# Kernel optimization log

Hardware: AMD Instinct MI355X
Metric: run time of the kernel (lower is better)

Reference implementation:

```python
import jax, jax.numpy as jnp
import numpy as np

B, N, DIM = 1, 4096, 512
HEADS, LOCAL_HEADS = 8, 4           # int(8*0.6)=4 local, 4 content
CONTENT_HEADS = HEADS - LOCAL_HEADS
HEAD_DIM = DIM // HEADS             # 64
WINDOW = 64                         # == H == W so window attention is well-formed
TOPK_RATIO = 0.2
SCALE = HEAD_DIM ** -0.5


def _window_partition(x, ws):
    Bb, H, W, C = x.shape
    pad_h = (ws - H % ws) % ws
    pad_w = (ws - W % ws) % ws
    x = jnp.pad(x, ((0, 0), (0, pad_h), (0, pad_w), (0, 0)))
    Hp, Wp = H + pad_h, W + pad_w
    x = x.reshape(Bb, Hp // ws, ws, Wp // ws, ws, C)
    win = x.transpose(0, 1, 3, 2, 4, 5).reshape(-1, ws, ws, C)
    return win, (Hp, Wp)


def _window_unpartition(win, ws, pad_hw, hw):
    Hp, Wp = pad_hw
    H, W = hw
    Bb = win.shape[0] // (Hp * Wp // ws // ws)
    x = win.reshape(Bb, Hp // ws, Wp // ws, ws, ws, -1)
    x = x.transpose(0, 1, 3, 2, 4, 5).reshape(Bb, Hp, Wp, -1)
    return x[:, :H, :W, :]


def setup_inputs() -> dict:
    key = jax.random.key(0)
    ks = jax.random.split(key, 12)
    s = 0.02
    f32 = jnp.float32
    ld = LOCAL_HEADS * HEAD_DIM      # 256
    cd = CONTENT_HEADS * HEAD_DIM    # 256
    return {
        'x': jax.random.normal(ks[0], (B, N, DIM), f32),
        'W_lqkv': jax.random.normal(ks[1], (DIM, 3 * ld), f32) * s,
        'b_lqkv': jnp.zeros((3 * ld,), f32),
        'W_cqkv': jax.random.normal(ks[2], (DIM, 3 * cd), f32) * s,
        'b_cqkv': jnp.zeros((3 * cd,), f32),
        'W_lproj': jax.random.normal(ks[3], (ld, DIM), f32) * s,
        'b_lproj': jnp.zeros((DIM,), f32),
        'W_cproj': jax.random.normal(ks[4], (cd, DIM), f32) * s,
        'b_cproj': jnp.zeros((DIM,), f32),
        'W_s1': jax.random.normal(ks[5], (DIM, DIM // 2), f32) * s,
        'b_s1': jnp.zeros((DIM // 2,), f32),
        'W_s2': jax.random.normal(ks[6], (DIM // 2, 1), f32) * s,
        'b_s2': jnp.zeros((1,), f32),
    }


def reference(x, W_lqkv, b_lqkv, W_cqkv, b_cqkv, W_lproj, b_lproj,
              W_cproj, b_cproj, W_s1, b_s1, W_s2, b_s2):
    Bb, Nn, C = x.shape
    H = W = int(np.sqrt(Nn))

    # ---- local (windowed) attention branch ----
    x_sp = x.reshape(Bb, H, W, C)
    x_win, pad_hw = _window_partition(x_sp, WINDOW)           # (Bw, ws, ws, C)
    Bw, Hw, Ww, _ = x_win.shape
    Nw = Hw * Ww
    xl = x_win.reshape(Bw, Nw, C)
    lqkv = (xl @ W_lqkv + b_lqkv).reshape(Bw, Nw, 3, LOCAL_HEADS, HEAD_DIM)
    lqkv = lqkv.transpose(2, 0, 3, 1, 4)                      # (3, Bw, h, Nw, d)
    lq, lk, lv = lqkv[0], lqkv[1], lqkv[2]
    lattn = jnp.einsum('bhqd,bhkd->bhqk', lq, lk) * SCALE
    lattn = jax.nn.softmax(lattn, axis=-1)
    lo = jnp.einsum('bhqk,bhkd->bhqd', lattn, lv)
    lo = lo.transpose(0, 2, 1, 3).reshape(Bw, Hw, Ww, LOCAL_HEADS * HEAD_DIM)
    lo = _window_unpartition(lo, WINDOW, pad_hw, (H, W)).reshape(Bb, Nn, -1)
    local_x = lo @ W_lproj + b_lproj

    # ---- saliency-gated content-based sparse attention branch ----
    h = jax.nn.gelu(x @ W_s1 + b_s1, approximate=False)
    scores = (h @ W_s2 + b_s2)[..., 0]                        # (B, N)
    K = max(1, int(Nn * TOPK_RATIO))
    _, idx = jax.lax.top_k(scores, K)                         # (B, K)
    mask = jnp.zeros((Bb, Nn), bool).at[jnp.arange(Bb)[:, None], idx].set(True)

    cqkv = (x @ W_cqkv + b_cqkv).reshape(Bb, Nn, 3, CONTENT_HEADS, HEAD_DIM)
    cqkv = cqkv.transpose(2, 0, 3, 1, 4)
    cq, ck, cv = cqkv[0], cqkv[1], cqkv[2]
    cattn = jnp.einsum('bhqd,bhkd->bhqk', cq, ck) * SCALE
    cattn = jnp.where(mask[:, None, None, :], cattn, -jnp.inf)
    cattn = jax.nn.softmax(cattn, axis=-1)
    co = jnp.einsum('bhqk,bhkd->bhqd', cattn, cv)
    co = co.transpose(0, 2, 1, 3).reshape(Bb, Nn, CONTENT_HEADS * HEAD_DIM)
    content_x = co @ W_cproj + b_cproj

    out = local_x + content_x
    attn = jnp.concatenate([lattn.mean(axis=1), cattn.mean(axis=1)], axis=1)
    return out, attn
```

## Files before the change

kernel.cpp:

```cpp
#include <hip/hip_runtime.h>

typedef __bf16 bf16;
typedef __bf16 bf16x8 __attribute__((ext_vector_type(8)));
typedef float  floatx4 __attribute__((ext_vector_type(4)));

#define SCALE 0.125f

__device__ __forceinline__ floatx4 mfma16(bf16x8 a, bf16x8 b, floatx4 c) {
    return __builtin_amdgcn_mfma_f32_16x16x32_bf16(a, b, c, 0, 0, 0);
}

__device__ __forceinline__ bf16x8 load_f32_as_bf16x8(const float* p) {
    float4 f0 = *(const float4*)p;
    float4 f1 = *(const float4*)(p + 4);
    bf16x8 a;
    a[0] = (bf16)f0.x; a[1] = (bf16)f0.y; a[2] = (bf16)f0.z; a[3] = (bf16)f0.w;
    a[4] = (bf16)f1.x; a[5] = (bf16)f1.y; a[6] = (bf16)f1.z; a[7] = (bf16)f1.w;
    return a;
}

__global__ void k_transpose(const float* __restrict__ src, bf16* __restrict__ dst,
                            int R, int C) {
    __shared__ float tile[32][33];
    int c0 = blockIdx.x * 32, r0 = blockIdx.y * 32;
    int tx = threadIdx.x, ty = threadIdx.y;
    for (int i = ty; i < 32; i += 8) {
        int r = r0 + i, c = c0 + tx;
        tile[i][tx] = (r < R && c < C) ? src[r * C + c] : 0.f;
    }
    __syncthreads();
    for (int i = ty; i < 32; i += 8) {
        int r = r0 + tx, c = c0 + i;
        if (r < R && c < C) dst[(size_t)c * R + r] = (bf16)tile[tx][i];
    }
}

__global__ __launch_bounds__(256) void k_qkv(
    const float* __restrict__ x,
    const bf16* __restrict__ WlT, const bf16* __restrict__ WcT,
    const float* __restrict__ b_l, const float* __restrict__ b_c,
    bf16* __restrict__ lq, bf16* __restrict__ lk, bf16* __restrict__ lvT,
    bf16* __restrict__ cq, bf16* __restrict__ ck, bf16* __restrict__ cv)
{
    const int tid = threadIdx.x;
    const int wave = tid >> 6, lane = tid & 63;
    const int ln15 = lane & 15, quad = lane >> 4;
    const int m0 = blockIdx.x * 64 + wave * 16;
    const int n0 = blockIdx.y * 64;

    floatx4 acc[4];
    for (int s = 0; s < 4; ++s) acc[s] = (floatx4){0.f, 0.f, 0.f, 0.f};

    for (int k0 = 0; k0 < 512; k0 += 32) {
        bf16x8 a = load_f32_as_bf16x8(x + (m0 + ln15) * 512 + k0 + quad * 8);
        for (int s = 0; s < 4; ++s) {
            int cg = n0 + s * 16 + ln15;
            const bf16* bt = (cg < 768) ? (WlT + cg * 512) : (WcT + (cg - 768) * 512);
            bf16x8 b = *(const bf16x8*)(bt + k0 + quad * 8);
            acc[s] = mfma16(a, b, acc[s]);
        }
    }

    for (int s = 0; s < 4; ++s) {
        int cg = n0 + s * 16 + ln15;
        for (int r = 0; r < 4; ++r) {
            int row = m0 + quad * 4 + r;
            float v = acc[s][r];
            if (cg < 768) {
                v += b_l[cg];
                int qkv = cg >> 8, hh = (cg >> 6) & 3, d = cg & 63;
                bf16 bv = (bf16)v;
                if (qkv == 0)      lq[(hh * 4096 + row) * 64 + d] = bv;
                else if (qkv == 1) lk[(hh * 4096 + row) * 64 + d] = bv;
                else               lvT[(hh * 64 + d) * 4096 + row] = bv;
            } else {
                int c = cg - 768;
                v += b_c[c];
                int qkv = c >> 8, hh = (c >> 6) & 3, d = c & 63;
                bf16 bv = (bf16)v;
                if (qkv == 0)      cq[(hh * 4096 + row) * 64 + d] = bv;
                else if (qkv == 1) ck[(hh * 4096 + row) * 64 + d] = bv;
                else               cv[(hh * 4096 + row) * 64 + d] = bv;
            }
        }
    }
}

__global__ __launch_bounds__(256) void k_scores(
    const float* __restrict__ x, const float* __restrict__ Ws1,
    const float* __restrict__ bs1, const float* __restrict__ Ws2,
    const float* __restrict__ bs2, float* __restrict__ scores)
{
    __shared__ float xs[4][512];
    int row0 = blockIdx.x * 4;
    int t = threadIdx.x;
    for (int i = t; i < 512; i += 256) {
        int r = i >> 7, k4 = (i & 127) * 4;
        *(float4*)&xs[r][k4] = *(const float4*)&x[(row0 + r) * 512 + k4];
    }
    __syncthreads();
    int r = t >> 6, cb = (t & 63) * 4;
    float acc[4] = {0.f, 0.f, 0.f, 0.f};
    #pragma unroll 4
    for (int k = 0; k < 512; ++k) {
        float a = xs[r][k];
        float4 w = *(const float4*)(Ws1 + k * 256 + cb);
        acc[0] = fmaf(a, w.x, acc[0]); acc[1] = fmaf(a, w.y, acc[1]);
        acc[2] = fmaf(a, w.z, acc[2]); acc[3] = fmaf(a, w.w, acc[3]);
    }
    float s = 0.f;
    for (int j = 0; j < 4; ++j) {
        float v = acc[j] + bs1[cb + j];
        float g = 0.5f * v * (1.0f + erff(v * 0.70710678118654752f));
        s = fmaf(g, Ws2[cb + j], s);
    }
    s += __shfl_xor(s, 1, 64);  s += __shfl_xor(s, 2, 64);
    s += __shfl_xor(s, 4, 64);  s += __shfl_xor(s, 8, 64);
    s += __shfl_xor(s, 16, 64); s += __shfl_xor(s, 32, 64);
    if ((t & 63) == 0) scores[row0 + r] = s + bs2[0];
}

__global__ __launch_bounds__(1024) void k_topk(const float* __restrict__ scores,
                                               int* __restrict__ sel, int* __restrict__ pos) {
    __shared__ unsigned long long key[4096];
    int tid = threadIdx.x;
    for (int i = tid; i < 4096; i += 1024) {
        unsigned u = __float_as_uint(scores[i]);
        u = (u & 0x80000000u) ? ~u : (u | 0x80000000u);
        key[i] = ((unsigned long long)u << 32) | (unsigned)(~i);
        pos[i] = -1;
    }
    __syncthreads();
    for (int k = 2; k <= 4096; k <<= 1) {
        for (int j = k >> 1; j > 0; j >>= 1) {
            for (int i = tid; i < 4096; i += 1024) {
                int ixj = i ^ j;
                if (ixj > i) {
                    unsigned long long a = key[i], b = key[ixj];
                    bool desc = (i & k) == 0;
                    if (desc ? (a < b) : (a > b)) { key[i] = b; key[ixj] = a; }
                }
            }
            __syncthreads();
        }
    }
    for (int r = tid; r < 819; r += 1024) {
        int idx = (int)(~(unsigned)(key[r] & 0xFFFFFFFFu));
        sel[r] = idx;
        pos[idx] = r;
    }
}

__global__ __launch_bounds__(256) void k_gather(
    const bf16* __restrict__ ck, const bf16* __restrict__ cv,
    const int* __restrict__ sel,
    bf16* __restrict__ ckg, bf16* __restrict__ cvgT)
{
    int g = blockIdx.x * 4 + (threadIdx.x >> 6);
    int d = threadIdx.x & 63;
    int hh = g / 896, r = g % 896;
    int src = (r < 819) ? sel[r] : -1;
    bf16 kv = (src >= 0) ? ck[(hh * 4096 + src) * 64 + d] : (bf16)0.0f;
    bf16 vv = (src >= 0) ? cv[(hh * 4096 + src) * 64 + d] : (bf16)0.0f;
    ckg[(hh * 896 + r) * 64 + d] = kv;
    cvgT[(hh * 64 + d) * 896 + r] = vv;
}

__global__ __launch_bounds__(256) void k_zero(uint4* __restrict__ p, int n) {
    int i = blockIdx.x * 256 + threadIdx.x;
    if (i < n) p[i] = (uint4){0u, 0u, 0u, 0u};
}

__global__ __launch_bounds__(256) void k_pass1(
    const bf16* __restrict__ lq, const bf16* __restrict__ lk,
    const bf16* __restrict__ cq, const bf16* __restrict__ ckg,
    float* __restrict__ lsum) {
    int wave = threadIdx.x >> 6, lane = threadIdx.x & 63;
    int ln15 = lane & 15, quad = lane >> 4;
    int y = blockIdx.y;
    int m0 = blockIdx.x * 64 + wave * 16;
    bool local = y < 32;
    int h    = local ? (y >> 3) : ((y - 32) >> 1);
    int kbeg = local ? (y & 7) * 512 : ((y - 32) & 1) * 416;
    int kcnt = local ? 512 : 416;
    const bf16* Q  = local ? lq + h * 4096 * 64 : cq + h * 4096 * 64;
    const bf16* Kt = local ? lk + h * 4096 * 64 : ckg + h * 896 * 64;
    int lsbase = (local ? h : 4 + h) * 4096;

    bf16x8 a0 = *(const bf16x8*)(Q + (m0 + ln15) * 64 + quad * 8);
    bf16x8 a1 = *(const bf16x8*)(Q + (m0 + ln15) * 64 + 32 + quad * 8);
    float se[4] = {0.f, 0.f, 0.f, 0.f};

    #pragma unroll 2
    for (int key0 = kbeg; key0 < kbeg + kcnt; key0 += 16) {
        const bf16* krow = Kt + (key0 + ln15) * 64;
        floatx4 z = (floatx4){0.f, 0.f, 0.f, 0.f};
        z = mfma16(a0, *(const bf16x8*)(krow + quad * 8), z);
        z = mfma16(a1, *(const bf16x8*)(krow + 32 + quad * 8), z);
        bool valid = local || (key0 + ln15) < 819;
        if (valid)
            for (int r = 0; r < 4; ++r) se[r] += __expf(fminf(z[r] * SCALE, 60.f));
    }
    for (int r = 0; r < 4; ++r) {
        float s = se[r];
        s += __shfl_xor(s, 1, 64);
        s += __shfl_xor(s, 2, 64);
        s += __shfl_xor(s, 4, 64);
        s += __shfl_xor(s, 8, 64);
        if (ln15 == 0) atomicAdd(&lsum[lsbase + m0 + quad * 4 + r], s);
    }
}

__global__ __launch_bounds__(256) void k_pass2(
    const bf16* __restrict__ lq, const bf16* __restrict__ lk, const bf16* __restrict__ lvT,
    const bf16* __restrict__ cq, const bf16* __restrict__ ckg, const bf16* __restrict__ cvgT,
    const float* __restrict__ lsum,
    float* __restrict__ attn_local,
    bf16* __restrict__ pcomp,
    float* __restrict__ lo,
    float* __restrict__ co)
{
    __shared__ __align__(16) bf16 pbuf[4][4][16 * 40];
    int wave = threadIdx.x >> 6, lane = threadIdx.x & 63;
    int ln15 = lane & 15, quad = lane >> 4;
    int tile = blockIdx.x, y = blockIdx.y;
    int m0 = tile * 64 + wave * 16;
    bool local = y < 16;
    const bf16* Q  = local ? lq : cq;
    const bf16* Kt = local ? lk : ckg;
    const bf16* Vt = local ? lvT : cvgT;
    int NV = local ? 4096 : 896;
    int kbeg = local ? y * 256 : (y - 16) * 224;
    int kend = kbeg + (local ? 256 : 224);
    int hbase = local ? 0 : 4;

    bf16x8 af[4][2];
    for (int h2 = 0; h2 < 4; ++h2)
        for (int ks = 0; ks < 2; ++ks)
            af[h2][ks] = *(const bf16x8*)(Q + (h2 * 4096 + m0 + ln15) * 64 + ks * 32 + quad * 8);

    float rl[4][4];
    for (int h2 = 0; h2 < 4; ++h2)
        for (int r = 0; r < 4; ++r)
            rl[h2][r] = 1.0f / fmaxf(lsum[(hbase + h2) * 4096 + m0 + quad * 4 + r], 1e-30f);

    floatx4 o[4][4];
    for (int h2 = 0; h2 < 4; ++h2)
        for (int ds = 0; ds < 4; ++ds) o[h2][ds] = (floatx4){0.f, 0.f, 0.f, 0.f};

    for (int key0 = kbeg; key0 < kend; key0 += 32) {
        float pm[2][4] = {{0.f, 0.f, 0.f, 0.f}, {0.f, 0.f, 0.f, 0.f}};
        #pragma unroll
        for (int h2 = 0; h2 < 4; ++h2) {
            bf16* pb = &pbuf[wave][h2][0];
            for (int s = 0; s < 2; ++s) {
                int kc = key0 + s * 16;
                const bf16* krow = Kt + (h2 * NV + kc + ln15) * 64;
                floatx4 z = (floatx4){0.f, 0.f, 0.f, 0.f};
                z = mfma16(af[h2][0], *(const bf16x8*)(krow + quad * 8), z);
                z = mfma16(af[h2][1], *(const bf16x8*)(krow + 32 + quad * 8), z);
                bool valid = local || (kc + ln15) < 819;
                for (int r = 0; r < 4; ++r) {
                    float p = valid ? __expf(fminf(z[r] * SCALE, 60.f)) * rl[h2][r] : 0.0f;
                    pm[s][r] += p;
                    pb[(quad * 4 + r) * 40 + s * 16 + ln15] = (bf16)p;
                }
            }
            bf16x8 ap = *(const bf16x8*)(pb + ln15 * 40 + quad * 8);
            for (int ds = 0; ds < 4; ++ds) {
                const bf16* vrow = Vt + (h2 * 64 + ds * 16 + ln15) * NV + key0 + quad * 8;
                o[h2][ds] = mfma16(ap, *(const bf16x8*)vrow, o[h2][ds]);
            }
        }
        if (local) {
            for (int s = 0; s < 2; ++s)
                for (int r = 0; r < 4; ++r)
                    attn_local[(m0 + quad * 4 + r) * 4096 + key0 + s * 16 + ln15] =
                        pm[s][r] * 0.25f;
        } else {
            for (int s = 0; s < 2; ++s) {
                int kc = key0 + s * 16 + ln15;
                if (kc < 832)
                    for (int r = 0; r < 4; ++r)
                        pcomp[(m0 + quad * 4 + r) * 832 + kc] = (bf16)(pm[s][r] * 0.25f);
            }
        }
    }

    float* ob = local ? lo : co;
    for (int h2 = 0; h2 < 4; ++h2)
        for (int ds = 0; ds < 4; ++ds)
            for (int r = 0; r < 4; ++r)
                atomicAdd(&ob[(m0 + quad * 4 + r) * 256 + h2 * 64 + ds * 16 + ln15],
                          o[h2][ds][r]);
}

__global__ __launch_bounds__(256) void k_expand(const bf16* __restrict__ pcomp,
                                                const int* __restrict__ pos,
                                                float* __restrict__ attn_content) {
    int row = blockIdx.x;
    int c0 = threadIdx.x * 16;
    const bf16* prow = pcomp + row * 832;
    float vals[16];
    #pragma unroll
    for (int j = 0; j < 16; ++j) {
        int p = pos[c0 + j];
        vals[j] = (p >= 0) ? (float)prow[p] : 0.0f;
    }
    float* dst = attn_content + (size_t)row * 4096 + c0;
    *(float4*)(dst)      = (float4){vals[0], vals[1], vals[2], vals[3]};
    *(float4*)(dst + 4)  = (float4){vals[4], vals[5], vals[6], vals[7]};
    *(float4*)(dst + 8)  = (float4){vals[8], vals[9], vals[10], vals[11]};
    *(float4*)(dst + 12) = (float4){vals[12], vals[13], vals[14], vals[15]};
}

__global__ __launch_bounds__(256) void k_proj(
    const float* __restrict__ lo, const float* __restrict__ co,
    const bf16* __restrict__ WlpT, const bf16* __restrict__ WcpT,
    const float* __restrict__ bl, const float* __restrict__ bc,
    float* __restrict__ out)
{
    const int tid = threadIdx.x;
    const int wave = tid >> 6, lane = tid & 63;
    const int ln15 = lane & 15, quad = lane >> 4;
    const int m0 = blockIdx.x * 64 + wave * 16;
    const int n0 = blockIdx.y * 64;

    floatx4 acc[4];
    for (int s = 0; s < 4; ++s) acc[s] = (floatx4){0.f, 0.f, 0.f, 0.f};

    for (int k0 = 0; k0 < 256; k0 += 32) {
        bf16x8 al = load_f32_as_bf16x8(lo + (m0 + ln15) * 256 + k0 + quad * 8);
        bf16x8 ac = load_f32_as_bf16x8(co + (m0 + ln15) * 256 + k0 + quad * 8);
        for (int s = 0; s < 4; ++s) {
            int c = n0 + s * 16 + ln15;
            acc[s] = mfma16(al, *(const bf16x8*)(WlpT + c * 256 + k0 + quad * 8), acc[s]);
            acc[s] = mfma16(ac, *(const bf16x8*)(WcpT + c * 256 + k0 + quad * 8), acc[s]);
        }
    }
    for (int s = 0; s < 4; ++s) {
        int c = n0 + s * 16 + ln15;
        float bias = bl[c] + bc[c];
        for (int r = 0; r < 4; ++r)
            out[(m0 + quad * 4 + r) * 512 + c] = acc[s][r] + bias;
    }
}

#define OFF_WLQKVT  0L
#define OFF_WCQKVT  786432L
#define OFF_LQ      1572864L
#define OFF_LK      3670016L
#define OFF_LVT     5767168L
#define OFF_CQ      7864320L
#define OFF_CK      9961472L
#define OFF_CV      12058624L
#define OFF_PCOMP   9961472L
#define OFF_CKG     16777216L
#define OFF_CVGT    17235968L
#define OFF_WLPT    16777216L
#define OFF_WCPT    17039360L
#define OFF_SCORES  17694720L
#define OFF_SEL     17711104L
#define OFF_POS     17715200L
#define OFF_LSUM    17731584L
#define OFF_LO      17862656L
#define OFF_CO      22056960L
#define WS_TOTAL    26251264L

extern "C" void kernel_launch(void* const* d_in, const int* in_sizes, int n_in,
                              void* d_out, int out_size, void* d_ws, size_t ws_size,
                              hipStream_t stream) {
    if (ws_size < (size_t)WS_TOTAL) return;

    const float* x       = (const float*)d_in[0];
    const float* W_lqkv  = (const float*)d_in[1];
    const float* b_lqkv  = (const float*)d_in[2];
    const float* W_cqkv  = (const float*)d_in[3];
    const float* b_cqkv  = (const float*)d_in[4];
    const float* W_lproj = (const float*)d_in[5];
    const float* b_lproj = (const float*)d_in[6];
    const float* W_cproj = (const float*)d_in[7];
    const float* b_cproj = (const float*)d_in[8];
    const float* W_s1    = (const float*)d_in[9];
    const float* b_s1    = (const float*)d_in[10];
    const float* W_s2    = (const float*)d_in[11];
    const float* b_s2    = (const float*)d_in[12];

    char* ws = (char*)d_ws;
    bf16* WlqkvT  = (bf16*)(ws + OFF_WLQKVT);
    bf16* WcqkvT  = (bf16*)(ws + OFF_WCQKVT);
    bf16* lq    = (bf16*)(ws + OFF_LQ);
    bf16* lk    = (bf16*)(ws + OFF_LK);
    bf16* lvT   = (bf16*)(ws + OFF_LVT);
    bf16* cq    = (bf16*)(ws + OFF_CQ);
    bf16* ck    = (bf16*)(ws + OFF_CK);
    bf16* cv    = (bf16*)(ws + OFF_CV);
    bf16* pcomp = (bf16*)(ws + OFF_PCOMP);
    bf16* ckg   = (bf16*)(ws + OFF_CKG);
    bf16* cvgT  = (bf16*)(ws + OFF_CVGT);
    bf16* WlpT  = (bf16*)(ws + OFF_WLPT);
    bf16* WcpT  = (bf16*)(ws + OFF_WCPT);
    float* scores  = (float*)(ws + OFF_SCORES);
    int*   sel     = (int*)(ws + OFF_SEL);
    int*   pos     = (int*)(ws + OFF_POS);
    float* lsum    = (float*)(ws + OFF_LSUM);
    float* lo      = (float*)(ws + OFF_LO);
    float* co      = (float*)(ws + OFF_CO);

    float* outp = (float*)d_out;
    float* attn_local   = outp + 2097152;
    float* attn_content = attn_local + 4096 * 4096;

    k_transpose<<<dim3(24, 16), dim3(32, 8), 0, stream>>>(W_lqkv, WlqkvT, 512, 768);
    k_transpose<<<dim3(24, 16), dim3(32, 8), 0, stream>>>(W_cqkv, WcqkvT, 512, 768);

    k_qkv<<<dim3(64, 24), 256, 0, stream>>>(x, WlqkvT, WcqkvT, b_lqkv, b_cqkv,
                                            lq, lk, lvT, cq, ck, cv);
    k_scores<<<1024, 256, 0, stream>>>(x, W_s1, b_s1, W_s2, b_s2, scores);
    k_topk<<<1, 1024, 0, stream>>>(scores, sel, pos);
    k_gather<<<896, 256, 0, stream>>>(ck, cv, sel, ckg, cvgT);
    k_zero<<<2080, 256, 0, stream>>>((uint4*)(ws + OFF_LSUM), 532480);
    k_pass1<<<dim3(64, 40), 256, 0, stream>>>(lq, lk, cq, ckg, lsum);
    k_pass2<<<dim3(64, 20), 256, 0, stream>>>(lq, lk, lvT, cq, ckg, cvgT, lsum,
                                              attn_local, pcomp, lo, co);
    k_transpose<<<dim3(16, 8), dim3(32, 8), 0, stream>>>(W_lproj, WlpT, 256, 512);
    k_transpose<<<dim3(16, 8), dim3(32, 8), 0, stream>>>(W_cproj, WcpT, 256, 512);
    k_expand<<<4096, 256, 0, stream>>>(pcomp, pos, attn_content);
    k_proj<<<dim3(64, 8), 256, 0, stream>>>(lo, co, WlpT, WcpT, b_lproj, b_cproj, outp);
}
```

Baseline: 733.1 us.

## Split pass2 into attention-map kernel and per-head PV kernel without atomics

The fused pass2 kernel, which wrote attention-map averages and accumulated P·V through atomics across key-split blocks, is split into two kernels. pass2a only recomputes the probabilities and writes the head-averaged attention maps. pass2b gives each block one head and the full key range, so it writes lo/co directly with normalization applied at the end. Dropping the atomics means lo/co no longer need zeroing, so the zero kernel shrinks to cover only lsum. In exchange, QK^T and exp are recomputed in both kernels, and pass2b has fewer, longer-running blocks (512), which may lower parallelism.

```diff
diff --git a/kernel.cpp b/kernel.cpp
--- a/kernel.cpp
+++ b/kernel.cpp
@@ -211,48 +211,42 @@
     }
 }
 
-__global__ __launch_bounds__(256) void k_pass2(
-    const bf16* __restrict__ lq, const bf16* __restrict__ lk, const bf16* __restrict__ lvT,
-    const bf16* __restrict__ cq, const bf16* __restrict__ ckg, const bf16* __restrict__ cvgT,
+__global__ __launch_bounds__(256) void k_pass2a(
+    const bf16* __restrict__ lq, const bf16* __restrict__ lk,
+    const bf16* __restrict__ cq, const bf16* __restrict__ ckg,
     const float* __restrict__ lsum,
     float* __restrict__ attn_local,
-    bf16* __restrict__ pcomp,
-    float* __restrict__ lo,
-    float* __restrict__ co)
-{
-    __shared__ __align__(16) bf16 pbuf[4][4][16 * 40];
+    bf16* __restrict__ pcomp)
+{
     int wave = threadIdx.x >> 6, lane = threadIdx.x & 63;
     int ln15 = lane & 15, quad = lane >> 4;
-    int tile = blockIdx.x, y = blockIdx.y;
-    int m0 = tile * 64 + wave * 16;
+    int m0 = blockIdx.x * 64 + wave * 16;
+    int y = blockIdx.y;
     bool local = y < 16;
     const bf16* Q  = local ? lq : cq;
     const bf16* Kt = local ? lk : ckg;
-    const bf16* Vt = local ? lvT : cvgT;
     int NV = local ? 4096 : 896;
     int kbeg = local ? y * 256 : (y - 16) * 224;
     int kend = kbeg + (local ? 256 : 224);
     int hbase = local ? 0 : 4;
 
     bf16x8 af[4][2];
+    #pragma unroll
     for (int h2 = 0; h2 < 4; ++h2)
         for (int ks = 0; ks < 2; ++ks)
             af[h2][ks] = *(const bf16x8*)(Q + (h2 * 4096 + m0 + ln15) * 64 + ks * 32 + quad * 8);
 
     float rl[4][4];
+    #pragma unroll
     for (int h2 = 0; h2 < 4; ++h2)
         for (int r = 0; r < 4; ++r)
-            rl[h2][r] = 1.0f / fmaxf(lsum[(hbase + h2) * 4096 + m0 + quad * 4 + r], 1e-30f);
-
-    floatx4 o[4][4];
-    for (int h2 = 0; h2 < 4; ++h2)
-        for (int ds = 0; ds < 4; ++ds) o[h2][ds] = (floatx4){0.f, 0.f, 0.f, 0.f};
+            rl[h2][r] = 0.25f / fmaxf(lsum[(hbase + h2) * 4096 + m0 + quad * 4 + r], 1e-30f);
 
     for (int key0 = kbeg; key0 < kend; key0 += 32) {
         float pm[2][4] = {{0.f, 0.f, 0.f, 0.f}, {0.f, 0.f, 0.f, 0.f}};
         #pragma unroll
         for (int h2 = 0; h2 < 4; ++h2) {
-            bf16* pb = &pbuf[wave][h2][0];
+            #pragma unroll
             for (int s = 0; s < 2; ++s) {
                 int kc = key0 + s * 16;
                 const bf16* krow = Kt + (h2 * NV + kc + ln15) * 64;
@@ -260,39 +254,95 @@
                 z = mfma16(af[h2][0], *(const bf16x8*)(krow + quad * 8), z);
                 z = mfma16(af[h2][1], *(const bf16x8*)(krow + 32 + quad * 8), z);
                 bool valid = local || (kc + ln15) < 819;
-                for (int r = 0; r < 4; ++r) {
-                    float p = valid ? __expf(fminf(z[r] * SCALE, 60.f)) * rl[h2][r] : 0.0f;
-                    pm[s][r] += p;
-                    pb[(quad * 4 + r) * 40 + s * 16 + ln15] = (bf16)p;
-                }
+                if (valid)
+                    for (int r = 0; r < 4; ++r)
+                        pm[s][r] += __expf(fminf(z[r] * SCALE, 60.f)) * rl[h2][r];
             }
-            bf16x8 ap = *(const bf16x8*)(pb + ln15 * 40 + quad * 8);
-            for (int ds = 0; ds < 4; ++ds) {
-                const bf16* vrow = Vt + (h2 * 64 + ds * 16 + ln15) * NV + key0 + quad * 8;
-                o[h2][ds] = mfma16(ap, *(const bf16x8*)vrow, o[h2][ds]);
-            }
         }
         if (local) {
+            #pragma unroll
             for (int s = 0; s < 2; ++s)
                 for (int r = 0; r < 4; ++r)
-                    attn_local[(m0 + quad * 4 + r) * 4096 + key0 + s * 16 + ln15] =
-                        pm[s][r] * 0.25f;
+                    attn_local[(m0 + quad * 4 + r) * 4096 + key0 + s * 16 + ln15] = pm[s][r];
         } else {
+            #pragma unroll
             for (int s = 0; s < 2; ++s) {
                 int kc = key0 + s * 16 + ln15;
                 if (kc < 832)
                     for (int r = 0; r < 4; ++r)
-                        pcomp[(m0 + quad * 4 + r) * 832 + kc] = (bf16)(pm[s][r] * 0.25f);
+                        pcomp[(m0 + quad * 4 + r) * 832 + kc] = (bf16)pm[s][r];
             }
         }
     }
+}
+
+__global__ __launch_bounds__(256) void k_pass2b(
+    const bf16* __restrict__ lq, const bf16* __restrict__ lk, const bf16* __restrict__ lvT,
+    const bf16* __restrict__ cq, const bf16* __restrict__ ckg, const bf16* __restrict__ cvgT,
+    const float* __restrict__ lsum,
+    float* __restrict__ lo,
+    float* __restrict__ co)
+{
+    __shared__ __align__(16) bf16 pbuf[4][2][16 * 40];
+    int wave = threadIdx.x >> 6, lane = threadIdx.x & 63;
+    int ln15 = lane & 15, quad = lane >> 4;
+    int m0 = blockIdx.x * 64 + wave * 16;
+    int y = blockIdx.y;
+    bool local = y < 4;
+    int h = local ? y : y - 4;
+    const bf16* Q  = local ? lq : cq;
+    const bf16* Kt = local ? lk : ckg;
+    const bf16* Vt = local ? lvT : cvgT;
+    int NV = local ? 4096 : 896;
+    int kcnt = local ? 4096 : 896;
+    int hbase = local ? 0 : 4;
+
+    const bf16* Qh = Q + (h * 4096 + m0) * 64;
+    const bf16* Kh = Kt + h * NV * 64;
+    const bf16* Vh = Vt + h * 64 * NV;
+
+    bf16x8 af0 = *(const bf16x8*)(Qh + ln15 * 64 + quad * 8);
+    bf16x8 af1 = *(const bf16x8*)(Qh + ln15 * 64 + 32 + quad * 8);
+
+    floatx4 o[4];
+    #pragma unroll
+    for (int ds = 0; ds < 4; ++ds) o[ds] = (floatx4){0.f, 0.f, 0.f, 0.f};
+
+    #pragma unroll 2
+    for (int key0 = 0; key0 < kcnt; key0 += 32) {
+        bf16* pb = &pbuf[wave][(key0 >> 5) & 1][0];
+        #pragma unroll
+        for (int s = 0; s < 2; ++s) {
+            int kc = key0 + s * 16;
+            const bf16* krow = Kh + (kc + ln15) * 64;
+            floatx4 z = (floatx4){0.f, 0.f, 0.f, 0.f};
+            z = mfma16(af0, *(const bf16x8*)(krow + quad * 8), z);
+            z = mfma16(af1, *(const bf16x8*)(krow + 32 + quad * 8), z);
+            bool valid = local || (kc + ln15) < 819;
+            #pragma unroll
+            for (int r = 0; r < 4; ++r) {
+                float p = valid ? __expf(fminf(z[r] * SCALE, 60.f)) : 0.0f;
+                pb[(quad * 4 + r) * 40 + s * 16 + ln15] = (bf16)p;
+            }
+        }
+        bf16x8 ap = *(const bf16x8*)(pb + ln15 * 40 + quad * 8);
+        #pragma unroll
+        for (int ds = 0; ds < 4; ++ds) {
+            const bf16* vrow = Vh + (ds * 16 + ln15) * NV + key0 + quad * 8;
+            o[ds] = mfma16(ap, *(const bf16x8*)vrow, o[ds]);
+        }
+    }
+
+    float rl[4];
+    #pragma unroll
+    for (int r = 0; r < 4; ++r)
+        rl[r] = 1.0f / fmaxf(lsum[(hbase + h) * 4096 + m0 + quad * 4 + r], 1e-30f);
 
     float* ob = local ? lo : co;
-    for (int h2 = 0; h2 < 4; ++h2)
-        for (int ds = 0; ds < 4; ++ds)
-            for (int r = 0; r < 4; ++r)
-                atomicAdd(&ob[(m0 + quad * 4 + r) * 256 + h2 * 64 + ds * 16 + ln15],
-                          o[h2][ds][r]);
+    #pragma unroll
+    for (int ds = 0; ds < 4; ++ds)
+        for (int r = 0; r < 4; ++r)
+            ob[(m0 + quad * 4 + r) * 256 + h * 64 + ds * 16 + ln15] = o[ds][r] * rl[r];
 }
 
 __global__ __launch_bounds__(256) void k_expand(const bf16* __restrict__ pcomp,
@@ -419,10 +469,11 @@
     k_scores<<<1024, 256, 0, stream>>>(x, W_s1, b_s1, W_s2, b_s2, scores);
     k_topk<<<1, 1024, 0, stream>>>(scores, sel, pos);
     k_gather<<<896, 256, 0, stream>>>(ck, cv, sel, ckg, cvgT);
-    k_zero<<<2080, 256, 0, stream>>>((uint4*)(ws + OFF_LSUM), 532480);
+    k_zero<<<32, 256, 0, stream>>>((uint4*)(ws + OFF_LSUM), 8192);
     k_pass1<<<dim3(64, 40), 256, 0, stream>>>(lq, lk, cq, ckg, lsum);
-    k_pass2<<<dim3(64, 20), 256, 0, stream>>>(lq, lk, lvT, cq, ckg, cvgT, lsum,
-                                              attn_local, pcomp, lo, co);
+    k_pass2a<<<dim3(64, 20), 256, 0, stream>>>(lq, lk, cq, ckg, lsum,
+                                               attn_local, pcomp);
+    k_pass2b<<<dim3(64, 8), 256, 0, stream>>>(lq, lk, lvT, cq, ckg, cvgT, lsum, lo, co);
     k_transpose<<<dim3(16, 8), dim3(32, 8), 0, stream>>>(W_lproj, WlpT, 256, 512);
     k_transpose<<<dim3(16, 8), dim3(32, 8), 0, stream>>>(W_cproj, WcpT, 256, 512);
     k_expand<<<4096, 256, 0, stream>>>(pcomp, pos, attn_content);
```

Result: slower. 821.7 us (+12.1%).
